# Optimization experiments

Measured on AMD Instinct MI355X. Metric: run time of the kernel, lower is better.

## Reference

```python
import jax, jax.numpy as jnp
import numpy as np

DIM = 1024
HEADS = 16
DIM_HEAD = 64
INNER = HEADS * DIM_HEAD  # 1024
SCALE = DIM_HEAD ** -0.5


def setup_inputs() -> dict:
    key = jax.random.key(0)
    k1, k2, k3, k4 = jax.random.split(key, 4)
    B, N = 4, 2048
    x = jax.random.normal(k1, (B, N, DIM), dtype=jnp.float32)
    # Linear weights stored as [in, out] so y = x @ W (+ b)
    W_qkv = jax.random.normal(k2, (DIM, 3 * INNER), dtype=jnp.float32) * (DIM ** -0.5)
    W_out = jax.random.normal(k3, (INNER, DIM), dtype=jnp.float32) * (INNER ** -0.5)
    b_out = jax.random.normal(k4, (DIM,), dtype=jnp.float32) * 0.01
    return {"x": x, "W_qkv": W_qkv, "W_out": W_out, "b_out": b_out}


def reference(x, W_qkv, W_out, b_out):
    B, N, _ = x.shape
    qkv = x @ W_qkv  # [B, N, 3*INNER]
    q, k, v = jnp.split(qkv, 3, axis=-1)
    # [B, N, H, Dh] -> [B, H, N, Dh]
    reshape = lambda t: t.reshape(B, N, HEADS, DIM_HEAD).transpose(0, 2, 1, 3)
    q, k, v = reshape(q), reshape(k), reshape(v)
    dots = jnp.einsum("bhqd,bhkd->bhqk", q, k) * SCALE  # [B,H,N,N]
    attn = jax.nn.softmax(dots, axis=-1)
    out = jnp.einsum("bhqk,bhkd->bhqd", attn, v)  # [B,H,N,Dh]
    out = out.transpose(0, 2, 1, 3).reshape(B, N, INNER)
    return out @ W_out + b_out
```

## Files before the change

### kernel.cpp

```cpp
#include <hip/hip_runtime.h>


typedef _Float16 half8 __attribute__((ext_vector_type(8)));
typedef __fp16 fp16v2 __attribute__((ext_vector_type(2)));
typedef float floatx4 __attribute__((ext_vector_type(4)));
typedef unsigned short u16;

struct __align__(8) U16x4 { u16 x, y, z, w; };

__device__ __forceinline__ u16 f2h(float f) {
  union { _Float16 h; u16 u; } cv;
  cv.h = (_Float16)f;
  return cv.u;
}

__device__ __forceinline__ void g2l16(const void* g, void* l) {
  __builtin_amdgcn_global_load_lds(
      (const __attribute__((address_space(1))) void*)g,
      (__attribute__((address_space(3))) void*)l, 16, 0, 0);
}

__device__ __forceinline__ int swz(int c) { return (c & 3) ^ ((c >> 3) & 3); }
__device__ __forceinline__ int swz8(int s) { return (s & 7) ^ ((s >> 3) & 7); }

__global__ __launch_bounds__(256) void cast_f32_f16(const float* __restrict__ in,
                                                    u16* __restrict__ out) {
  long long base = ((long long)blockIdx.x * 256 + threadIdx.x) * 8;
  float4 a = *(const float4*)(in + base);
  float4 b = *(const float4*)(in + base + 4);
  U16x4 u0 = {f2h(a.x), f2h(a.y), f2h(a.z), f2h(a.w)};
  U16x4 u1 = {f2h(b.x), f2h(b.y), f2h(b.z), f2h(b.w)};
  *(U16x4*)(out + base) = u0;
  *(U16x4*)(out + base + 4) = u1;
}

__global__ __launch_bounds__(256) void transpose_cast(const float* __restrict__ in,
                                                      u16* __restrict__ out,
                                                      int K, int N) {
  __shared__ u16 ls[64][72];
  const int nTK = K >> 6;
  const int tk = blockIdx.x % nTK;
  const int tn = blockIdx.x / nTK;
  const int tid = threadIdx.x;
#pragma unroll
  for (int i = 0; i < 4; ++i) {
    int idx = i * 256 + tid;
    int r = idx >> 4, c4 = (idx & 15) * 4;
    float4 v = *(const float4*)(in + (long long)(tk * 64 + r) * N + tn * 64 + c4);
    ls[r][c4 + 0] = f2h(v.x);
    ls[r][c4 + 1] = f2h(v.y);
    ls[r][c4 + 2] = f2h(v.z);
    ls[r][c4 + 3] = f2h(v.w);
  }
  __syncthreads();
#pragma unroll
  for (int i = 0; i < 4; ++i) {
    int idx = i * 256 + tid;
    int nr = idx >> 4, kc4 = (idx & 15) * 4;
    U16x4 u = {ls[kc4 + 0][nr], ls[kc4 + 1][nr], ls[kc4 + 2][nr], ls[kc4 + 3][nr]};
    *(U16x4*)(out + (long long)(tn * 64 + nr) * K + tk * 64 + kc4) = u;
  }
}

template <int EPI>
__global__ __launch_bounds__(256, 4) void gemm_f16(const u16* __restrict__ A,
                                                   const u16* __restrict__ Bt,
                                                   u16* __restrict__ O0,
                                                   u16* __restrict__ O1,
                                                   u16* __restrict__ O2,
                                                   float* __restrict__ Of,
                                                   const float* __restrict__ bias) {
  __shared__ __attribute__((aligned(16))) u16 lsA[128 * 64];
  __shared__ __attribute__((aligned(16))) u16 lsB[128 * 64];
  const int tid = threadIdx.x;
  const int lane = tid & 63, wave = tid >> 6;
  const int l15 = lane & 15, quad = lane >> 4;
  const int w7 = l15 & 7;
  const int offk0 = ((quad) ^ w7) * 8;
  const int offk1 = ((4 + quad) ^ w7) * 8;
  const int wm = (wave >> 1) * 64, wn = (wave & 1) * 64;
  const int bm = blockIdx.x & 63;
  const int bn = blockIdx.x >> 6;

  const u16* ga[4];
  const u16* gb[4];
#pragma unroll
  for (int i = 0; i < 4; ++i) {
    int s = i * 256 + tid;
    ga[i] = A + (long long)(bm * 128 + (s >> 3)) * 1024 + swz8(s) * 8;
    gb[i] = Bt + (long long)(bn * 128 + (s >> 3)) * 1024 + swz8(s) * 8;
  }

  floatx4 acc[4][4] = {};

  for (int kt = 0; kt < 16; ++kt) {
    const int ko = kt * 64;
#pragma unroll
    for (int i = 0; i < 4; ++i)
      g2l16(ga[i] + ko, lsA + (i * 256 + wave * 64) * 8);
#pragma unroll
    for (int i = 0; i < 4; ++i)
      g2l16(gb[i] + ko, lsB + (i * 256 + wave * 64) * 8);
    __syncthreads();
#pragma unroll
    for (int ks = 0; ks < 2; ++ks) {
      const int off = ks ? offk1 : offk0;
      half8 af[4], bf[4];
#pragma unroll
      for (int mt = 0; mt < 4; ++mt)
        af[mt] = *(const half8*)(lsA + (wm + mt * 16 + l15) * 64 + off);
#pragma unroll
      for (int nt = 0; nt < 4; ++nt)
        bf[nt] = *(const half8*)(lsB + (wn + nt * 16 + l15) * 64 + off);
#pragma unroll
      for (int mt = 0; mt < 4; ++mt)
#pragma unroll
        for (int nt = 0; nt < 4; ++nt)
          acc[mt][nt] = __builtin_amdgcn_mfma_f32_16x16x32_f16(af[mt], bf[nt], acc[mt][nt], 0, 0, 0);
    }
    __syncthreads();
  }

  if (EPI == 0) {
    const float slq = 0.125f * 1.44269504088896f;
#pragma unroll
    for (int mt = 0; mt < 4; ++mt) {
      int gm = bm * 128 + wm + mt * 16 + quad * 4;
      int b = gm >> 11, n0 = gm & 2047;
#pragma unroll
      for (int nt = 0; nt < 4; ++nt) {
        int gc = bn * 128 + wn + nt * 16 + l15;
        int t = gc >> 10, hd = gc & 1023, h = hd >> 6, d = hd & 63;
        long long bh = (long long)(b * 16 + h);
        if (t == 2) {
          U16x4 u = {f2h(acc[mt][nt][0]), f2h(acc[mt][nt][1]),
                     f2h(acc[mt][nt][2]), f2h(acc[mt][nt][3])};
          *(U16x4*)(O2 + (bh * 64 + d) * 2048 + n0) = u;
        } else {
          float s = (t == 0) ? slq : 1.0f;
          u16* dst = (t == 0 ? O0 : O1) + (bh * 2048 + n0) * 64 + d;
#pragma unroll
          for (int r = 0; r < 4; ++r) dst[r * 64] = f2h(acc[mt][nt][r] * s);
        }
      }
    }
  } else {
#pragma unroll
    for (int mt = 0; mt < 4; ++mt) {
      int gm = bm * 128 + wm + mt * 16 + quad * 4;
#pragma unroll
      for (int nt = 0; nt < 4; ++nt) {
        int gc = bn * 128 + wn + nt * 16 + l15;
        float bv = bias[gc];
#pragma unroll
        for (int r = 0; r < 4; ++r)
          Of[(long long)(gm + r) * 1024 + gc] = acc[mt][nt][r] + bv;
      }
    }
  }
}

__global__ __launch_bounds__(256, 2) void attn_flash(const u16* __restrict__ Qh,
                                                     const u16* __restrict__ Kh,
                                                     const u16* __restrict__ Vt,
                                                     u16* __restrict__ Oh) {
  __shared__ __attribute__((aligned(16))) u16 lsK[2 * 2 * 64 * 32];
  __shared__ __attribute__((aligned(16))) u16 lsV[2 * 2 * 64 * 32];
  __shared__ __attribute__((aligned(16))) u16 lsP[4 * 64 * 32];
  const int tid = threadIdx.x;
  const int lane = tid & 63, wave = tid >> 6;
  const int l15 = lane & 15, quad = lane >> 4;
  const int sw = (l15 >> 1) & 3;
  const int qsw8 = (quad ^ sw) * 8;
  const int bh = blockIdx.x & 63, qt = blockIdx.x >> 6;
  const u16* Qb = Qh + ((long long)bh * 2048 + qt * 256) * 64;
  const u16* Kb = Kh + (long long)bh * 2048 * 64;
  const u16* Vb = Vt + (long long)bh * 64 * 2048;
  u16* lsPw = lsP + wave * 2048;

  half8 qb[4][2];
#pragma unroll
  for (int pass = 0; pass < 2; ++pass) {
#pragma unroll
    for (int i = 0; i < 4; ++i) {
      int c = i * 256 + tid;
      g2l16(Qb + (pass * 128 + ((c >> 2) & 127)) * 64 + (c >> 9) * 32 + swz(c) * 8,
            lsK + (i * 256 + wave * 64) * 8);
    }
    __syncthreads();
    if ((wave >> 1) == pass) {
      const int lrow = (wave & 1) * 64;
#pragma unroll
      for (int qt2 = 0; qt2 < 4; ++qt2)
#pragma unroll
        for (int ks = 0; ks < 2; ++ks)
          qb[qt2][ks] = *(const half8*)(lsK + ks * 4096 +
                                        (lrow + qt2 * 16 + l15) * 32 + qsw8);
    }
    __syncthreads();
  }

#pragma unroll
  for (int i = 0; i < 2; ++i) {
    int c = i * 256 + tid;
    g2l16(Kb + ((c >> 2) & 63) * 64 + (c >> 8) * 32 + swz(c) * 8,
          lsK + (i * 256 + wave * 64) * 8);
    g2l16(Vb + ((c >> 2) & 63) * 2048 + (c >> 8) * 32 + swz(c) * 8,
          lsV + (i * 256 + wave * 64) * 8);
  }

  half8 onesf;
#pragma unroll
  for (int j = 0; j < 8; ++j) onesf[j] = (_Float16)1.0f;

  floatx4 oacc[4][4] = {};
  floatx4 osum[4] = {};

  for (int kt = 0; kt < 32; ++kt) {
    const int cur = kt & 1;
    const u16* bufK = lsK + cur * 4096;
    const u16* bufV = lsV + cur * 4096;
    __syncthreads();
    if (kt < 31) {
      u16* nK = lsK + (1 - cur) * 4096;
      u16* nV = lsV + (1 - cur) * 4096;
#pragma unroll
      for (int i = 0; i < 2; ++i) {
        int c = i * 256 + tid;
        g2l16(Kb + (kt + 1) * 4096 + ((c >> 2) & 63) * 64 + (c >> 8) * 32 + swz(c) * 8,
              nK + (i * 256 + wave * 64) * 8);
        g2l16(Vb + ((c >> 2) & 63) * 2048 + (kt + 1) * 64 + (c >> 8) * 32 + swz(c) * 8,
              nV + (i * 256 + wave * 64) * 8);
      }
    }
#pragma unroll
    for (int ks4 = 0; ks4 < 2; ++ks4) {
      floatx4 sacc[2][4] = {};
#pragma unroll
      for (int ks = 0; ks < 2; ++ks) {
#pragma unroll
        for (int h = 0; h < 2; ++h) {
          half8 kf = *(const half8*)(bufK + ks * 2048 + ((ks4 * 2 + h) * 16 + l15) * 32 + qsw8);
#pragma unroll
          for (int qt2 = 0; qt2 < 4; ++qt2)
            sacc[h][qt2] = __builtin_amdgcn_mfma_f32_16x16x32_f16(kf, qb[qt2][ks], sacc[h][qt2], 0, 0, 0);
        }
      }
#pragma unroll
      for (int h = 0; h < 2; ++h) {
#pragma unroll
        for (int qt2 = 0; qt2 < 4; ++qt2) {
          float p0 = __builtin_amdgcn_exp2f(sacc[h][qt2][0]);
          float p1 = __builtin_amdgcn_exp2f(sacc[h][qt2][1]);
          float p2 = __builtin_amdgcn_exp2f(sacc[h][qt2][2]);
          float p3 = __builtin_amdgcn_exp2f(sacc[h][qt2][3]);
          union { fp16v2 h2; unsigned u; } lo, hi;
          lo.h2 = __builtin_amdgcn_cvt_pkrtz(p0, p1);
          hi.h2 = __builtin_amdgcn_cvt_pkrtz(p2, p3);
          uint2 pk = {lo.u, hi.u};
          *(uint2*)(lsPw + (qt2 * 16 + l15) * 32 +
                    (((2 * h + (quad >> 1)) ^ sw) * 8) + (quad & 1) * 4) = pk;
        }
      }
      half8 pa[4];
#pragma unroll
      for (int qt2 = 0; qt2 < 4; ++qt2)
        pa[qt2] = *(const half8*)(lsPw + (qt2 * 16 + l15) * 32 + qsw8);
#pragma unroll
      for (int dt = 0; dt < 4; ++dt) {
        half8 vb = *(const half8*)(bufV + ks4 * 2048 + (dt * 16 + l15) * 32 + qsw8);
#pragma unroll
        for (int qt2 = 0; qt2 < 4; ++qt2)
          oacc[qt2][dt] = __builtin_amdgcn_mfma_f32_16x16x32_f16(pa[qt2], vb, oacc[qt2][dt], 0, 0, 0);
      }
#pragma unroll
      for (int qt2 = 0; qt2 < 4; ++qt2)
        osum[qt2] = __builtin_amdgcn_mfma_f32_16x16x32_f16(pa[qt2], onesf, osum[qt2], 0, 0, 0);
    }
  }

  const int b = bh >> 4, h = bh & 15;
#pragma unroll
  for (int qt2 = 0; qt2 < 4; ++qt2) {
#pragma unroll
    for (int r = 0; r < 4; ++r) {
      float inv = 1.0f / osum[qt2][r];
      int qrow = qt * 256 + wave * 64 + qt2 * 16 + quad * 4 + r;
      long long rowbase = ((long long)b * 2048 + qrow) * 1024 + h * 64;
#pragma unroll
      for (int dt = 0; dt < 4; ++dt)
        Oh[rowbase + dt * 16 + l15] = f2h(oacc[qt2][dt][r] * inv);
    }
  }
}

extern "C" void kernel_launch(void* const* d_in, const int* in_sizes, int n_in,
                              void* d_out, int out_size, void* d_ws, size_t ws_size,
                              hipStream_t stream) {
  const float* x = (const float*)d_in[0];
  const float* Wqkv = (const float*)d_in[1];
  const float* Wout = (const float*)d_in[2];
  const float* bout = (const float*)d_in[3];
  float* out = (float*)d_out;

  char* ws = (char*)d_ws;
  u16* Xh = (u16*)(ws);
  u16* Wqkvt = (u16*)(ws + (16ll << 20));
  u16* Woutt = (u16*)(ws + (22ll << 20));
  u16* Qh = (u16*)(ws + (24ll << 20));
  u16* Kh = (u16*)(ws + (40ll << 20));
  u16* Vt = (u16*)(ws + (56ll << 20));
  u16* Oh = (u16*)(ws + (72ll << 20));

  cast_f32_f16<<<4096, 256, 0, stream>>>(x, Xh);
  transpose_cast<<<16 * 48, 256, 0, stream>>>(Wqkv, Wqkvt, 1024, 3072);
  transpose_cast<<<16 * 16, 256, 0, stream>>>(Wout, Woutt, 1024, 1024);
  gemm_f16<0><<<64 * 24, 256, 0, stream>>>(Xh, Wqkvt, Qh, Kh, Vt, nullptr, nullptr);
  attn_flash<<<512, 256, 0, stream>>>(Qh, Kh, Vt, Oh);
  gemm_f16<1><<<64 * 8, 256, 0, stream>>>(Oh, Woutt, nullptr, nullptr, nullptr, out, bout);
}
```

Measured before the change: 244.5 us.

## Rewrite GEMM as 8-wave 128x256 tile with 4-stage async LDS pipeline

Replaces the 4-wave 128x128 GEMM with an 8-wave kernel using a 128x256 block tile. It streams K in 32-wide slices through a 4-deep global_load_lds ring with manual vmcnt waits and a single barrier per step. Blocks are remapped to group tiles across XCDs, and s_setprio is raised around the MFMA bursts in both the GEMM and the attention kernel. The goal is to hide global load latency and cut per-iteration synchronisation, at the cost of hand-tuned wait counts that must stay exactly right.

```diff
diff --git a/kernel.cpp b/kernel.cpp
--- a/kernel.cpp
+++ b/kernel.cpp
@@ -21,7 +21,6 @@
 }
 
 __device__ __forceinline__ int swz(int c) { return (c & 3) ^ ((c >> 3) & 3); }
-__device__ __forceinline__ int swz8(int s) { return (s & 7) ^ ((s >> 3) & 7); }
 
 __global__ __launch_bounds__(256) void cast_f32_f16(const float* __restrict__ in,
                                                     u16* __restrict__ out) {
@@ -63,62 +62,80 @@
 }
 
 template <int EPI>
-__global__ __launch_bounds__(256, 4) void gemm_f16(const u16* __restrict__ A,
-                                                   const u16* __restrict__ Bt,
-                                                   u16* __restrict__ O0,
-                                                   u16* __restrict__ O1,
-                                                   u16* __restrict__ O2,
-                                                   float* __restrict__ Of,
-                                                   const float* __restrict__ bias) {
-  __shared__ __attribute__((aligned(16))) u16 lsA[128 * 64];
-  __shared__ __attribute__((aligned(16))) u16 lsB[128 * 64];
+__global__ __launch_bounds__(512, 2) void gemm8p(const u16* __restrict__ A,
+                                                 const u16* __restrict__ Bt,
+                                                 u16* __restrict__ O0,
+                                                 u16* __restrict__ O1,
+                                                 u16* __restrict__ O2,
+                                                 float* __restrict__ Of,
+                                                 const float* __restrict__ bias) {
+  __shared__ __attribute__((aligned(16))) u16 lsA[4 * 128 * 32];
+  __shared__ __attribute__((aligned(16))) u16 lsB[4 * 256 * 32];
   const int tid = threadIdx.x;
   const int lane = tid & 63, wave = tid >> 6;
   const int l15 = lane & 15, quad = lane >> 4;
-  const int w7 = l15 & 7;
-  const int offk0 = ((quad) ^ w7) * 8;
-  const int offk1 = ((4 + quad) ^ w7) * 8;
-  const int wm = (wave >> 1) * 64, wn = (wave & 1) * 64;
-  const int bm = blockIdx.x & 63;
-  const int bn = blockIdx.x >> 6;
-
-  const u16* ga[4];
-  const u16* gb[4];
-#pragma unroll
-  for (int i = 0; i < 4; ++i) {
-    int s = i * 256 + tid;
-    ga[i] = A + (long long)(bm * 128 + (s >> 3)) * 1024 + swz8(s) * 8;
-    gb[i] = Bt + (long long)(bn * 128 + (s >> 3)) * 1024 + swz8(s) * 8;
-  }
+  const int offAB = (quad ^ ((l15 >> 1) & 3)) * 8;
+  const int wm = (wave >> 2) * 64, wn = (wave & 3) * 64;
+  constexpr int nwg = (EPI == 0) ? 768 : 256;
+  const int b = (blockIdx.x & 7) * (nwg >> 3) + (blockIdx.x >> 3);
+  const int bm = b & 63, bn = b >> 6;
+
+  const int colsw = ((lane & 3) ^ ((lane >> 3) & 3)) * 8;
+  const u16* gA =
+      A + (long long)(bm * 128 + wave * 16 + (lane >> 2)) * 1024 + colsw;
+  const u16* gB[2];
+#pragma unroll
+  for (int i = 0; i < 2; ++i)
+    gB[i] = Bt + (long long)(bn * 256 + (wave * 2 + i) * 16 + (lane >> 2)) * 1024 +
+            colsw;
 
   floatx4 acc[4][4] = {};
 
-  for (int kt = 0; kt < 16; ++kt) {
-    const int ko = kt * 64;
-#pragma unroll
-    for (int i = 0; i < 4; ++i)
-      g2l16(ga[i] + ko, lsA + (i * 256 + wave * 64) * 8);
-#pragma unroll
-    for (int i = 0; i < 4; ++i)
-      g2l16(gb[i] + ko, lsB + (i * 256 + wave * 64) * 8);
-    __syncthreads();
-#pragma unroll
-    for (int ks = 0; ks < 2; ++ks) {
-      const int off = ks ? offk1 : offk0;
-      half8 af[4], bf[4];
-#pragma unroll
-      for (int mt = 0; mt < 4; ++mt)
-        af[mt] = *(const half8*)(lsA + (wm + mt * 16 + l15) * 64 + off);
+#pragma unroll
+  for (int j = 0; j < 3; ++j) {
+    g2l16(gA + j * 32, lsA + j * 4096 + wave * 512);
+#pragma unroll
+    for (int i = 0; i < 2; ++i)
+      g2l16(gB[i] + j * 32, lsB + j * 8192 + (wave * 2 + i) * 512);
+  }
+  asm volatile("s_waitcnt vmcnt(6)");
+  __builtin_amdgcn_s_barrier();
+
+  for (int kt = 0; kt < 32; ++kt) {
+    const int cb = kt & 3;
+    const u16* bA = lsA + cb * 4096;
+    const u16* bB = lsB + cb * 8192;
+    half8 af[4], bf[4];
+#pragma unroll
+    for (int mt = 0; mt < 4; ++mt)
+      af[mt] = *(const half8*)(bA + (wm + mt * 16 + l15) * 32 + offAB);
+#pragma unroll
+    for (int nt = 0; nt < 4; ++nt)
+      bf[nt] = *(const half8*)(bB + (wn + nt * 16 + l15) * 32 + offAB);
+    if (kt < 29) {
+      const int fb = (kt + 3) & 3;
+      g2l16(gA + (kt + 3) * 32, lsA + fb * 4096 + wave * 512);
+#pragma unroll
+      for (int i = 0; i < 2; ++i)
+        g2l16(gB[i] + (kt + 3) * 32, lsB + fb * 8192 + (wave * 2 + i) * 512);
+    }
+    __builtin_amdgcn_s_barrier();
+    asm volatile("s_waitcnt lgkmcnt(0)");
+    __builtin_amdgcn_s_setprio(1);
+#pragma unroll
+    for (int mt = 0; mt < 4; ++mt)
 #pragma unroll
       for (int nt = 0; nt < 4; ++nt)
-        bf[nt] = *(const half8*)(lsB + (wn + nt * 16 + l15) * 64 + off);
-#pragma unroll
-      for (int mt = 0; mt < 4; ++mt)
-#pragma unroll
-        for (int nt = 0; nt < 4; ++nt)
-          acc[mt][nt] = __builtin_amdgcn_mfma_f32_16x16x32_f16(af[mt], bf[nt], acc[mt][nt], 0, 0, 0);
-    }
-    __syncthreads();
+        acc[mt][nt] = __builtin_amdgcn_mfma_f32_16x16x32_f16(af[mt], bf[nt],
+                                                             acc[mt][nt], 0, 0, 0);
+    __builtin_amdgcn_s_setprio(0);
+    if (kt < 29)
+      asm volatile("s_waitcnt vmcnt(6)");
+    else if (kt == 29)
+      asm volatile("s_waitcnt vmcnt(3)");
+    else if (kt == 30)
+      asm volatile("s_waitcnt vmcnt(0)");
+    __builtin_amdgcn_s_barrier();
   }
 
   if (EPI == 0) {
@@ -126,12 +143,12 @@
 #pragma unroll
     for (int mt = 0; mt < 4; ++mt) {
       int gm = bm * 128 + wm + mt * 16 + quad * 4;
-      int b = gm >> 11, n0 = gm & 2047;
+      int bb = gm >> 11, n0 = gm & 2047;
 #pragma unroll
       for (int nt = 0; nt < 4; ++nt) {
-        int gc = bn * 128 + wn + nt * 16 + l15;
+        int gc = bn * 256 + wn + nt * 16 + l15;
         int t = gc >> 10, hd = gc & 1023, h = hd >> 6, d = hd & 63;
-        long long bh = (long long)(b * 16 + h);
+        long long bh = (long long)(bb * 16 + h);
         if (t == 2) {
           U16x4 u = {f2h(acc[mt][nt][0]), f2h(acc[mt][nt][1]),
                      f2h(acc[mt][nt][2]), f2h(acc[mt][nt][3])};
@@ -150,7 +167,7 @@
       int gm = bm * 128 + wm + mt * 16 + quad * 4;
 #pragma unroll
       for (int nt = 0; nt < 4; ++nt) {
-        int gc = bn * 128 + wn + nt * 16 + l15;
+        int gc = bn * 256 + wn + nt * 16 + l15;
         float bv = bias[gc];
 #pragma unroll
         for (int r = 0; r < 4; ++r)
@@ -236,6 +253,7 @@
 #pragma unroll
     for (int ks4 = 0; ks4 < 2; ++ks4) {
       floatx4 sacc[2][4] = {};
+      __builtin_amdgcn_s_setprio(1);
 #pragma unroll
       for (int ks = 0; ks < 2; ++ks) {
 #pragma unroll
@@ -246,6 +264,7 @@
             sacc[h][qt2] = __builtin_amdgcn_mfma_f32_16x16x32_f16(kf, qb[qt2][ks], sacc[h][qt2], 0, 0, 0);
         }
       }
+      __builtin_amdgcn_s_setprio(0);
 #pragma unroll
       for (int h = 0; h < 2; ++h) {
 #pragma unroll
@@ -266,6 +285,7 @@
 #pragma unroll
       for (int qt2 = 0; qt2 < 4; ++qt2)
         pa[qt2] = *(const half8*)(lsPw + (qt2 * 16 + l15) * 32 + qsw8);
+      __builtin_amdgcn_s_setprio(1);
 #pragma unroll
       for (int dt = 0; dt < 4; ++dt) {
         half8 vb = *(const half8*)(bufV + ks4 * 2048 + (dt * 16 + l15) * 32 + qsw8);
@@ -276,6 +296,7 @@
 #pragma unroll
       for (int qt2 = 0; qt2 < 4; ++qt2)
         osum[qt2] = __builtin_amdgcn_mfma_f32_16x16x32_f16(pa[qt2], onesf, osum[qt2], 0, 0, 0);
+      __builtin_amdgcn_s_setprio(0);
     }
   }
 
@@ -315,7 +336,7 @@
   cast_f32_f16<<<4096, 256, 0, stream>>>(x, Xh);
   transpose_cast<<<16 * 48, 256, 0, stream>>>(Wqkv, Wqkvt, 1024, 3072);
   transpose_cast<<<16 * 16, 256, 0, stream>>>(Wout, Woutt, 1024, 1024);
-  gemm_f16<0><<<64 * 24, 256, 0, stream>>>(Xh, Wqkvt, Qh, Kh, Vt, nullptr, nullptr);
+  gemm8p<0><<<768, 512, 0, stream>>>(Xh, Wqkvt, Qh, Kh, Vt, nullptr, nullptr);
   attn_flash<<<512, 256, 0, stream>>>(Qh, Kh, Vt, Oh);
-  gemm_f16<1><<<64 * 8, 256, 0, stream>>>(Oh, Woutt, nullptr, nullptr, nullptr, out, bout);
-}
+  gemm8p<1><<<256, 512, 0, stream>>>(Oh, Woutt, nullptr, nullptr, nullptr, out, bout);
+}
```

Result: slower. 270.2 us (+10.5%).

## Rewrite QKV and output GEMMs with larger tiles and double-buffered LDS pipeline

Applied to the files above, without the earlier changes.

Replaces the templated 128x128 single-buffered GEMM with two specialised kernels. The QKV kernel uses 256x256 tiles and the output kernel 256x128 tiles, both with 512 threads. Global-to-LDS loads for the next K step are issued alongside MFMA work on the current buffer, with split waitcnt and barrier sync and raised wave priority around the MFMA blocks. Block indices are remapped so neighbouring blocks share tiles in cache. The aim is to hide memory latency and improve data reuse, at the cost of more LDS and registers per block and fewer blocks in flight.

```diff
diff --git a/kernel.cpp b/kernel.cpp
--- a/kernel.cpp
+++ b/kernel.cpp
@@ -21,7 +21,6 @@
 }
 
 __device__ __forceinline__ int swz(int c) { return (c & 3) ^ ((c >> 3) & 3); }
-__device__ __forceinline__ int swz8(int s) { return (s & 7) ^ ((s >> 3) & 7); }
 
 __global__ __launch_bounds__(256) void cast_f32_f16(const float* __restrict__ in,
                                                     u16* __restrict__ out) {
@@ -62,100 +61,206 @@
   }
 }
 
-template <int EPI>
-__global__ __launch_bounds__(256, 4) void gemm_f16(const u16* __restrict__ A,
+__global__ __launch_bounds__(512, 2) void qkv_gemm(const u16* __restrict__ A,
                                                    const u16* __restrict__ Bt,
                                                    u16* __restrict__ O0,
                                                    u16* __restrict__ O1,
-                                                   u16* __restrict__ O2,
+                                                   u16* __restrict__ O2) {
+  __shared__ __attribute__((aligned(16))) u16 lsA[2 * 2 * 8192];
+  __shared__ __attribute__((aligned(16))) u16 lsB[2 * 2 * 8192];
+  const int tid = threadIdx.x;
+  const int lane = tid & 63, wid = tid >> 6;
+  const int l15 = lane & 15, quad = lane >> 4;
+  const int rdoff = (quad ^ ((l15 >> 1) & 3)) * 8;
+  const int wmrow = (wid >> 2) * 128, wnrow = (wid & 3) * 64;
+  const int b = (blockIdx.x & 7) * 48 + (blockIdx.x >> 3);
+  const int bm = b & 31, bn = b >> 5;
+
+  const u16* gAr[2];
+  const u16* gBr[2];
+#pragma unroll
+  for (int j = 0; j < 2; ++j) {
+    int sl = wid * 128 + j * 64 + lane;
+    int r = sl >> 2, cc = sl & 3;
+    int csw = cc ^ ((r >> 1) & 3);
+    gAr[j] = A + (long long)(bm * 256 + r) * 1024 + csw * 8;
+    gBr[j] = Bt + (long long)(bn * 256 + r) * 1024 + csw * 8;
+  }
+
+  floatx4 acc[8][4] = {};
+  half8 bf[4];
+
+#pragma unroll
+  for (int j = 0; j < 2; ++j) g2l16(gAr[j], lsA + (wid * 2 + j) * 512);
+#pragma unroll
+  for (int j = 0; j < 2; ++j) g2l16(gBr[j], lsB + (wid * 2 + j) * 512);
+#pragma unroll
+  for (int j = 0; j < 2; ++j) g2l16(gAr[j] + 32, lsA + 8192 + (wid * 2 + j) * 512);
+#pragma unroll
+  for (int j = 0; j < 2; ++j) g2l16(gBr[j] + 32, lsB + 8192 + (wid * 2 + j) * 512);
+  asm volatile("s_waitcnt vmcnt(4)");
+  __builtin_amdgcn_s_barrier();
+
+  for (int t = 0; t < 16; ++t) {
+    const int buf = t & 1;
+    const u16* bA = lsA + buf * 16384;
+    const u16* bB = lsB + buf * 16384;
+    u16* nA = lsA + (buf ^ 1) * 16384;
+    u16* nB = lsB + (buf ^ 1) * 16384;
+    const long long so = (long long)(t + 1) * 64;
+#pragma unroll
+    for (int p = 0; p < 4; ++p) {
+      const int ks = p >> 1, mh = p & 1, kh = p >> 1;
+      half8 af[4];
+#pragma unroll
+      for (int i = 0; i < 4; ++i)
+        af[i] = *(const half8*)(bA + ks * 8192 +
+                                (wmrow + mh * 64 + i * 16 + l15) * 32 + rdoff);
+      if (mh == 0) {
+#pragma unroll
+        for (int i = 0; i < 4; ++i)
+          bf[i] = *(const half8*)(bB + ks * 8192 + (wnrow + i * 16 + l15) * 32 + rdoff);
+      }
+      if (t < 15) {
+        if (mh == 0) {
+#pragma unroll
+          for (int j = 0; j < 2; ++j)
+            g2l16(gAr[j] + so + kh * 32, nA + kh * 8192 + (wid * 2 + j) * 512);
+        } else {
+#pragma unroll
+          for (int j = 0; j < 2; ++j)
+            g2l16(gBr[j] + so + kh * 32, nB + kh * 8192 + (wid * 2 + j) * 512);
+        }
+      }
+      __builtin_amdgcn_s_barrier();
+      asm volatile("s_waitcnt lgkmcnt(0)");
+      __builtin_amdgcn_s_setprio(1);
+#pragma unroll
+      for (int i = 0; i < 4; ++i)
+#pragma unroll
+        for (int nt = 0; nt < 4; ++nt)
+          acc[mh * 4 + i][nt] = __builtin_amdgcn_mfma_f32_16x16x32_f16(
+              af[i], bf[nt], acc[mh * 4 + i][nt], 0, 0, 0);
+      __builtin_amdgcn_s_setprio(0);
+      if (p == 1 || p == 3) {
+        if (t < 15) asm volatile("s_waitcnt vmcnt(4)");
+        else        asm volatile("s_waitcnt vmcnt(0)");
+      }
+      __builtin_amdgcn_s_barrier();
+    }
+  }
+
+  const float slq = 0.125f * 1.44269504088896f;
+#pragma unroll
+  for (int mt = 0; mt < 8; ++mt) {
+    int gm = bm * 256 + wmrow + mt * 16 + quad * 4;
+    int bb = gm >> 11, n0 = gm & 2047;
+#pragma unroll
+    for (int nt = 0; nt < 4; ++nt) {
+      int gc = bn * 256 + wnrow + nt * 16 + l15;
+      int tsel = gc >> 10, hd = gc & 1023, h = hd >> 6, d = hd & 63;
+      long long bh = (long long)(bb * 16 + h);
+      if (tsel == 2) {
+        U16x4 u = {f2h(acc[mt][nt][0]), f2h(acc[mt][nt][1]),
+                   f2h(acc[mt][nt][2]), f2h(acc[mt][nt][3])};
+        *(U16x4*)(O2 + (bh * 64 + d) * 2048 + n0) = u;
+      } else {
+        float s = (tsel == 0) ? slq : 1.0f;
+        u16* dst = (tsel == 0 ? O0 : O1) + (bh * 2048 + n0) * 64 + d;
+#pragma unroll
+        for (int r = 0; r < 4; ++r) dst[r * 64] = f2h(acc[mt][nt][r] * s);
+      }
+    }
+  }
+}
+
+__global__ __launch_bounds__(512, 2) void out_gemm(const u16* __restrict__ A,
+                                                   const u16* __restrict__ Bt,
                                                    float* __restrict__ Of,
                                                    const float* __restrict__ bias) {
-  __shared__ __attribute__((aligned(16))) u16 lsA[128 * 64];
-  __shared__ __attribute__((aligned(16))) u16 lsB[128 * 64];
+  __shared__ __attribute__((aligned(16))) u16 lsA[2 * 2 * 8192];
+  __shared__ __attribute__((aligned(16))) u16 lsB[2 * 2 * 4096];
   const int tid = threadIdx.x;
-  const int lane = tid & 63, wave = tid >> 6;
+  const int lane = tid & 63, wid = tid >> 6;
   const int l15 = lane & 15, quad = lane >> 4;
-  const int w7 = l15 & 7;
-  const int offk0 = ((quad) ^ w7) * 8;
-  const int offk1 = ((4 + quad) ^ w7) * 8;
-  const int wm = (wave >> 1) * 64, wn = (wave & 1) * 64;
-  const int bm = blockIdx.x & 63;
-  const int bn = blockIdx.x >> 6;
-
-  const u16* ga[4];
-  const u16* gb[4];
-#pragma unroll
-  for (int i = 0; i < 4; ++i) {
-    int s = i * 256 + tid;
-    ga[i] = A + (long long)(bm * 128 + (s >> 3)) * 1024 + swz8(s) * 8;
-    gb[i] = Bt + (long long)(bn * 128 + (s >> 3)) * 1024 + swz8(s) * 8;
+  const int rdoff = (quad ^ ((l15 >> 1) & 3)) * 8;
+  const int wmrow = (wid >> 1) * 64, wnrow = (wid & 1) * 64;
+  const int b = (blockIdx.x & 7) * 32 + (blockIdx.x >> 3);
+  const int bm = b & 31, bn = b >> 5;
+
+  const u16* gAr[2];
+#pragma unroll
+  for (int j = 0; j < 2; ++j) {
+    int sl = wid * 128 + j * 64 + lane;
+    int r = sl >> 2, cc = sl & 3;
+    gAr[j] = A + (long long)(bm * 256 + r) * 1024 + (cc ^ ((r >> 1) & 3)) * 8;
+  }
+  const u16* gBr;
+  {
+    int sl = wid * 64 + lane;
+    int r = sl >> 2, cc = sl & 3;
+    gBr = Bt + (long long)(bn * 128 + r) * 1024 + (cc ^ ((r >> 1) & 3)) * 8;
   }
 
   floatx4 acc[4][4] = {};
 
-  for (int kt = 0; kt < 16; ++kt) {
-    const int ko = kt * 64;
-#pragma unroll
-    for (int i = 0; i < 4; ++i)
-      g2l16(ga[i] + ko, lsA + (i * 256 + wave * 64) * 8);
-#pragma unroll
-    for (int i = 0; i < 4; ++i)
-      g2l16(gb[i] + ko, lsB + (i * 256 + wave * 64) * 8);
-    __syncthreads();
-#pragma unroll
-    for (int ks = 0; ks < 2; ++ks) {
-      const int off = ks ? offk1 : offk0;
+#pragma unroll
+  for (int j = 0; j < 2; ++j) g2l16(gAr[j], lsA + (wid * 2 + j) * 512);
+  g2l16(gBr, lsB + wid * 512);
+#pragma unroll
+  for (int j = 0; j < 2; ++j) g2l16(gAr[j] + 32, lsA + 8192 + (wid * 2 + j) * 512);
+  g2l16(gBr + 32, lsB + 4096 + wid * 512);
+  asm volatile("s_waitcnt vmcnt(3)");
+  __builtin_amdgcn_s_barrier();
+
+  for (int t = 0; t < 16; ++t) {
+    const int buf = t & 1;
+    const u16* bA = lsA + buf * 16384;
+    const u16* bB = lsB + buf * 8192;
+    u16* nA = lsA + (buf ^ 1) * 16384;
+    u16* nB = lsB + (buf ^ 1) * 8192;
+    const long long so = (long long)(t + 1) * 64;
+#pragma unroll
+    for (int p = 0; p < 2; ++p) {
       half8 af[4], bf[4];
 #pragma unroll
-      for (int mt = 0; mt < 4; ++mt)
-        af[mt] = *(const half8*)(lsA + (wm + mt * 16 + l15) * 64 + off);
-#pragma unroll
-      for (int nt = 0; nt < 4; ++nt)
-        bf[nt] = *(const half8*)(lsB + (wn + nt * 16 + l15) * 64 + off);
-#pragma unroll
-      for (int mt = 0; mt < 4; ++mt)
+      for (int i = 0; i < 4; ++i)
+        af[i] = *(const half8*)(bA + p * 8192 + (wmrow + i * 16 + l15) * 32 + rdoff);
+#pragma unroll
+      for (int i = 0; i < 4; ++i)
+        bf[i] = *(const half8*)(bB + p * 4096 + (wnrow + i * 16 + l15) * 32 + rdoff);
+      if (t < 15) {
+#pragma unroll
+        for (int j = 0; j < 2; ++j)
+          g2l16(gAr[j] + so + p * 32, nA + p * 8192 + (wid * 2 + j) * 512);
+        g2l16(gBr + so + p * 32, nB + p * 4096 + wid * 512);
+      }
+      __builtin_amdgcn_s_barrier();
+      asm volatile("s_waitcnt lgkmcnt(0)");
+      __builtin_amdgcn_s_setprio(1);
+#pragma unroll
+      for (int i = 0; i < 4; ++i)
 #pragma unroll
         for (int nt = 0; nt < 4; ++nt)
-          acc[mt][nt] = __builtin_amdgcn_mfma_f32_16x16x32_f16(af[mt], bf[nt], acc[mt][nt], 0, 0, 0);
-    }
-    __syncthreads();
-  }
-
-  if (EPI == 0) {
-    const float slq = 0.125f * 1.44269504088896f;
-#pragma unroll
-    for (int mt = 0; mt < 4; ++mt) {
-      int gm = bm * 128 + wm + mt * 16 + quad * 4;
-      int b = gm >> 11, n0 = gm & 2047;
-#pragma unroll
-      for (int nt = 0; nt < 4; ++nt) {
-        int gc = bn * 128 + wn + nt * 16 + l15;
-        int t = gc >> 10, hd = gc & 1023, h = hd >> 6, d = hd & 63;
-        long long bh = (long long)(b * 16 + h);
-        if (t == 2) {
-          U16x4 u = {f2h(acc[mt][nt][0]), f2h(acc[mt][nt][1]),
-                     f2h(acc[mt][nt][2]), f2h(acc[mt][nt][3])};
-          *(U16x4*)(O2 + (bh * 64 + d) * 2048 + n0) = u;
-        } else {
-          float s = (t == 0) ? slq : 1.0f;
-          u16* dst = (t == 0 ? O0 : O1) + (bh * 2048 + n0) * 64 + d;
-#pragma unroll
-          for (int r = 0; r < 4; ++r) dst[r * 64] = f2h(acc[mt][nt][r] * s);
-        }
-      }
-    }
-  } else {
-#pragma unroll
-    for (int mt = 0; mt < 4; ++mt) {
-      int gm = bm * 128 + wm + mt * 16 + quad * 4;
-#pragma unroll
-      for (int nt = 0; nt < 4; ++nt) {
-        int gc = bn * 128 + wn + nt * 16 + l15;
-        float bv = bias[gc];
-#pragma unroll
-        for (int r = 0; r < 4; ++r)
-          Of[(long long)(gm + r) * 1024 + gc] = acc[mt][nt][r] + bv;
-      }
+          acc[i][nt] = __builtin_amdgcn_mfma_f32_16x16x32_f16(af[i], bf[nt],
+                                                              acc[i][nt], 0, 0, 0);
+      __builtin_amdgcn_s_setprio(0);
+      if (t < 15) asm volatile("s_waitcnt vmcnt(3)");
+      else        asm volatile("s_waitcnt vmcnt(0)");
+      __builtin_amdgcn_s_barrier();
+    }
+  }
+
+#pragma unroll
+  for (int mt = 0; mt < 4; ++mt) {
+    int gm = bm * 256 + wmrow + mt * 16 + quad * 4;
+#pragma unroll
+    for (int nt = 0; nt < 4; ++nt) {
+      int gc = bn * 128 + wnrow + nt * 16 + l15;
+      float bv = bias[gc];
+#pragma unroll
+      for (int r = 0; r < 4; ++r)
+        Of[(long long)(gm + r) * 1024 + gc] = acc[mt][nt][r] + bv;
     }
   }
 }
@@ -315,7 +420,7 @@
   cast_f32_f16<<<4096, 256, 0, stream>>>(x, Xh);
   transpose_cast<<<16 * 48, 256, 0, stream>>>(Wqkv, Wqkvt, 1024, 3072);
   transpose_cast<<<16 * 16, 256, 0, stream>>>(Wout, Woutt, 1024, 1024);
-  gemm_f16<0><<<64 * 24, 256, 0, stream>>>(Xh, Wqkvt, Qh, Kh, Vt, nullptr, nullptr);
+  qkv_gemm<<<384, 512, 0, stream>>>(Xh, Wqkvt, Qh, Kh, Vt);
   attn_flash<<<512, 256, 0, stream>>>(Qh, Kh, Vt, Oh);
-  gemm_f16<1><<<64 * 8, 256, 0, stream>>>(Oh, Woutt, nullptr, nullptr, nullptr, out, bout);
-}
+  out_gemm<<<256, 512, 0, stream>>>(Oh, Woutt, out, bout);
+}
```

After: 294.8 us. 1.21x slower.
